# Performance work log

Hardware: AMD Instinct MI355X
Metric: run time of the kernel (lower is better)

## Reference

```python
import jax, jax.numpy as jnp
import numpy as np

N_NODES = 100000


def setup_inputs() -> dict:
    key = jax.random.key(0)
    k_x, k_e, k_w1, k_b1, k_w2, k_b2 = jax.random.split(key, 6)
    num_features, hidden, num_classes = 128, 64, 32
    x = jax.random.normal(k_x, (N_NODES, num_features), dtype=jnp.float32)
    edge_index = jax.random.randint(k_e, (2, 1600000), 0, N_NODES, dtype=jnp.int64)
    # torch.nn.Linear default init: U(-1/sqrt(fan_in), 1/sqrt(fan_in))
    s1 = 1.0 / np.sqrt(num_features)
    s2 = 1.0 / np.sqrt(hidden)
    W1 = jax.random.uniform(k_w1, (num_features, hidden), jnp.float32, -s1, s1)
    b1 = jax.random.uniform(k_b1, (hidden,), jnp.float32, -s1, s1)
    W2 = jax.random.uniform(k_w2, (hidden, num_classes), jnp.float32, -s2, s2)
    b2 = jax.random.uniform(k_b2, (num_classes,), jnp.float32, -s2, s2)
    return {"x": x, "edge_index": edge_index, "W1": W1, "b1": b1, "W2": W2, "b2": b2}


def reference(x, edge_index, W1, b1, W2, b2):
    # GNNConv: linear then scatter-add aggregation with self-loops
    xl = x @ W1 + b1                      # [N, hidden]
    src, dst = edge_index[0], edge_index[1]
    msgs = xl[src]                        # gather source features [E, hidden]
    agg = jax.ops.segment_sum(msgs, dst, num_segments=N_NODES)
    agg = agg + xl                        # add_self_loops contributes xl to each node
    h = jax.nn.relu(agg)
    return h @ W2 + b2                    # [N, num_classes]
```

## Files before the change

kernel.cpp:

```cpp
#include <hip/hip_runtime.h>
#include <hip/hip_bf16.h>

#define TPB 256
#define BSHIFT 7
#define BNODES (1 << BSHIFT)
#define NWRITERS 256

typedef int vint4 __attribute__((ext_vector_type(4)));
typedef __attribute__((ext_vector_type(8))) short short8v;
typedef __attribute__((ext_vector_type(4))) float f32x4;

__device__ __forceinline__ unsigned short f2bf(float f) {
    unsigned int u = __float_as_uint(f);
    u += 0x7fffu + ((u >> 16) & 1u);
    return (unsigned short)(u >> 16);
}
__device__ __forceinline__ float bflo(unsigned int u) { return __uint_as_float(u << 16); }
__device__ __forceinline__ float bfhi(unsigned int u) { return __uint_as_float(u & 0xffff0000u); }

__global__ __launch_bounds__(TPB) void k_gemm1_hist(
    const float* __restrict__ x, const float* __restrict__ W1, const float* __restrict__ b1,
    unsigned int* __restrict__ xlb,
    const int* __restrict__ ei, int* __restrict__ cntT,
    int N, int E, int NB, int CH)
{
    __shared__ unsigned short wT[64 * 136];
    __shared__ float b1s[64];
    __shared__ int   lcnt[1024];

    const int t = threadIdx.x;

    if ((int)blockIdx.x < NWRITERS) {
        const int hb = blockIdx.x;
        const int start = hb * CH;
        const int lim = min(E, start + CH);
        for (int j = t; j < NB; j += TPB) lcnt[j] = 0;
        __syncthreads();
        const int* dst = ei + E;
        int i = start + t * 4;
        for (; i + 3 < lim; i += TPB * 4) {
            vint4 d = __builtin_nontemporal_load(reinterpret_cast<const vint4*>(dst + i));
            atomicAdd(&lcnt[d.x >> BSHIFT], 1);
            atomicAdd(&lcnt[d.y >> BSHIFT], 1);
            atomicAdd(&lcnt[d.z >> BSHIFT], 1);
            atomicAdd(&lcnt[d.w >> BSHIFT], 1);
        }
        for (i = start + ((lim - start) & ~3) + t; i < lim; i += TPB)
            atomicAdd(&lcnt[dst[i] >> BSHIFT], 1);
        __syncthreads();
        for (int j = t; j < NB; j += TPB) cntT[j * NWRITERS + hb] = lcnt[j];
        return;
    }

    for (int i = t; i < 2048; i += TPB) {
        int k = i >> 4, cw = (i & 15) * 4;
        float4 u = reinterpret_cast<const float4*>(W1)[i];
        wT[(cw + 0) * 136 + k] = f2bf(u.x);
        wT[(cw + 1) * 136 + k] = f2bf(u.y);
        wT[(cw + 2) * 136 + k] = f2bf(u.z);
        wT[(cw + 3) * 136 + k] = f2bf(u.w);
    }
    if (t < 64) b1s[t] = b1[t];
    __syncthreads();

    const int l = t & 63, wid = t >> 6;
    const int cl = l & 15, kg = l >> 4;
    const int rw = ((int)blockIdx.x - NWRITERS) * 64 + wid * 16;
    if (rw >= N) return;
    const int r = rw + cl;

    const float4* xp4 = reinterpret_cast<const float4*>(x) + ((size_t)min(r, N - 1) * 32 + kg * 2);

    f32x4 acc[4] = {};
    #pragma unroll
    for (int kt = 0; kt < 4; ++kt) {
        float4 fA = xp4[kt * 8];
        float4 fB = xp4[kt * 8 + 1];
        short8v a;
        a[0] = (short)f2bf(fA.x); a[1] = (short)f2bf(fA.y);
        a[2] = (short)f2bf(fA.z); a[3] = (short)f2bf(fA.w);
        a[4] = (short)f2bf(fB.x); a[5] = (short)f2bf(fB.y);
        a[6] = (short)f2bf(fB.z); a[7] = (short)f2bf(fB.w);
        #pragma unroll
        for (int ct = 0; ct < 4; ++ct) {
            short8v b = *reinterpret_cast<const short8v*>(
                &wT[(ct * 16 + cl) * 136 + kt * 32 + kg * 8]);
            acc[ct] = __builtin_amdgcn_mfma_f32_16x16x32_bf16(a, b, acc[ct], 0, 0, 0);
        }
    }

    #pragma unroll
    for (int ct = 0; ct < 4; ++ct) {
        #pragma unroll
        for (int reg = 0; reg < 4; ++reg) {
            int row = rw + kg * 4 + reg;
            float v = acc[ct][reg] + b1s[ct * 16 + cl];
            unsigned int m = (unsigned int)f2bf(v);
            unsigned int p = (unsigned int)__shfl_xor((int)m, 1);
            if (!(l & 1) && row < N)
                xlb[(size_t)row * 32 + ct * 8 + (cl >> 1)] = m | (p << 16);
        }
    }
}

__global__ __launch_bounds__(TPB) void k_colscan(
    const int* __restrict__ cntT, int* __restrict__ segT, int* __restrict__ totals, int NB)
{
    __shared__ int wsum[4];
    const int r = blockIdx.x;
    const int t = threadIdx.x;
    const int lane = t & 63, wid = t >> 6;
    int v = cntT[r * NWRITERS + t];
    int incl = v;
    for (int d = 1; d < 64; d <<= 1) {
        int n = __shfl_up(incl, d);
        if (lane >= d) incl += n;
    }
    if (lane == 63) wsum[wid] = incl;
    __syncthreads();
    int woff = 0;
    for (int w = 0; w < wid; w++) woff += wsum[w];
    int excl = woff + incl - v;
    segT[r * NWRITERS + t] = excl;
    if (t == TPB - 1) totals[r] = excl + v;
}

__global__ void k_bucketbase(const int* __restrict__ totals, int* __restrict__ bb, int NB, int E)
{
    const int lane = threadIdx.x & 63;
    int carry = 0;
    for (int it = 0; it * 64 < NB; ++it) {
        int idx = it * 64 + lane;
        int v = (idx < NB) ? totals[idx] : 0;
        int incl = v;
        for (int d = 1; d < 64; d <<= 1) {
            int n = __shfl_up(incl, d);
            if (lane >= d) incl += n;
        }
        if (idx < NB) bb[idx] = carry + incl - v;
        carry += __shfl(incl, 63);
    }
    if (lane == 0) bb[NB] = E;
}

__global__ __launch_bounds__(TPB) void k_fillbin(
    const int* __restrict__ ei, const int* __restrict__ segT, const int* __restrict__ bb,
    unsigned int* __restrict__ recs, int E, int NB, int CH)
{
    __shared__ int lcur[1024];
    const int blk = blockIdx.x;
    const int t = threadIdx.x;
    for (int j = t; j < NB; j += TPB)
        lcur[j] = bb[j] + segT[j * NWRITERS + blk];
    __syncthreads();

    const int start = blk * CH;
    const int lim = min(E, start + CH);
    const int* src = ei;
    const int* dst = ei + E;
    int i = start + t * 4;
    for (; i + 3 < lim; i += TPB * 4) {
        vint4 d = __builtin_nontemporal_load(reinterpret_cast<const vint4*>(dst + i));
        vint4 s = __builtin_nontemporal_load(reinterpret_cast<const vint4*>(src + i));
        int p0 = atomicAdd(&lcur[d.x >> BSHIFT], 1);
        int p1 = atomicAdd(&lcur[d.y >> BSHIFT], 1);
        int p2 = atomicAdd(&lcur[d.z >> BSHIFT], 1);
        int p3 = atomicAdd(&lcur[d.w >> BSHIFT], 1);
        recs[p0] = ((unsigned int)s.x << BSHIFT) | (unsigned int)(d.x & (BNODES-1));
        recs[p1] = ((unsigned int)s.y << BSHIFT) | (unsigned int)(d.y & (BNODES-1));
        recs[p2] = ((unsigned int)s.z << BSHIFT) | (unsigned int)(d.z & (BNODES-1));
        recs[p3] = ((unsigned int)s.w << BSHIFT) | (unsigned int)(d.w & (BNODES-1));
    }
    for (i = start + ((lim - start) & ~3) + t; i < lim; i += TPB) {
        int d = dst[i];
        int p = atomicAdd(&lcur[d >> BSHIFT], 1);
        recs[p] = ((unsigned int)src[i] << BSHIFT) | (unsigned int)(d & (BNODES-1));
    }
}

__global__ __launch_bounds__(TPB) void k_bsort(
    const unsigned int* __restrict__ recs, const int* __restrict__ bb,
    int* __restrict__ esrc, int* __restrict__ off, int N, int NB, int E)
{
    __shared__ int h[BNODES];
    __shared__ int cur[BNODES];
    __shared__ int ws2[2];

    const int r = blockIdx.x;
    const int t = threadIdx.x;
    const int bb0 = bb[r], bb1 = bb[r + 1];

    if (t < BNODES) h[t] = 0;
    __syncthreads();
    for (int i = bb0 + t; i < bb1; i += TPB)
        atomicAdd(&h[recs[i] & (BNODES - 1)], 1);
    __syncthreads();

    int v = 0, incl = 0;
    const int lane = t & 63, w = t >> 6;
    if (t < BNODES) {
        v = h[t];
        incl = v;
        for (int d = 1; d < 64; d <<= 1) {
            int n = __shfl_up(incl, d);
            if (lane >= d) incl += n;
        }
        if (lane == 63) ws2[w] = incl;
    }
    __syncthreads();
    if (t < BNODES) {
        int excl = incl - v + (w ? ws2[0] : 0);
        cur[t] = bb0 + excl;
        int node = r * BNODES + t;
        if (node < N) off[node] = bb0 + excl;
    }
    if (r == NB - 1 && t == 0) off[N] = E;
    __syncthreads();

    for (int i = bb0 + t; i < bb1; i += TPB) {
        unsigned int rec = recs[i];
        int p = atomicAdd(&cur[rec & (BNODES - 1)], 1);
        esrc[p] = (int)(rec >> BSHIFT);
    }
}

#define AGG_BLOCKS 2048
__global__ __launch_bounds__(TPB) void k_agg(
    const unsigned int* __restrict__ xlb,
    const int* __restrict__ off,
    const int* __restrict__ esrc,
    const float* __restrict__ W2,
    const float* __restrict__ b2,
    float* __restrict__ out, int N)
{
    __shared__ float w2s[64 * 32];
    __shared__ float b2s[32];
    __shared__ float arow[4][68];

    const int t = threadIdx.x;
    const float4* w4 = reinterpret_cast<const float4*>(W2);
    for (int i = t; i < 512; i += TPB) {
        float4 u = w4[i];
        int o = i * 4;
        w2s[o+0] = u.x; w2s[o+1] = u.y; w2s[o+2] = u.z; w2s[o+3] = u.w;
    }
    if (t < 32) b2s[t] = b2[t];
    __syncthreads();

    const int wid = t >> 6, lane = t & 63;
    const int slot = lane >> 4, b = lane & 15;
    const int c = lane & 31, h = lane >> 5;
    const uint2* xb2 = reinterpret_cast<const uint2*>(xlb);

    for (int node = blockIdx.x * 4 + wid; node < N; node += gridDim.x * 4) {
        const int beg = off[node], end = off[node + 1];
        float a0 = 0.f, a1 = 0.f, a2 = 0.f, a3 = 0.f;
        int e = beg + slot;
        for (; e + 12 < end; e += 16) {
            int s0 = esrc[e], s1 = esrc[e + 4], s2 = esrc[e + 8], s3 = esrc[e + 12];
            uint2 v0 = xb2[(size_t)s0 * 16 + b];
            uint2 v1 = xb2[(size_t)s1 * 16 + b];
            uint2 v2 = xb2[(size_t)s2 * 16 + b];
            uint2 v3 = xb2[(size_t)s3 * 16 + b];
            a0 += bflo(v0.x); a1 += bfhi(v0.x); a2 += bflo(v0.y); a3 += bfhi(v0.y);
            a0 += bflo(v1.x); a1 += bfhi(v1.x); a2 += bflo(v1.y); a3 += bfhi(v1.y);
            a0 += bflo(v2.x); a1 += bfhi(v2.x); a2 += bflo(v2.y); a3 += bfhi(v2.y);
            a0 += bflo(v3.x); a1 += bfhi(v3.x); a2 += bflo(v3.y); a3 += bfhi(v3.y);
        }
        for (; e < end; e += 4) {
            uint2 v = xb2[(size_t)esrc[e] * 16 + b];
            a0 += bflo(v.x); a1 += bfhi(v.x); a2 += bflo(v.y); a3 += bfhi(v.y);
        }
        a0 += __shfl_xor(a0, 16); a1 += __shfl_xor(a1, 16);
        a2 += __shfl_xor(a2, 16); a3 += __shfl_xor(a3, 16);
        a0 += __shfl_xor(a0, 32); a1 += __shfl_xor(a1, 32);
        a2 += __shfl_xor(a2, 32); a3 += __shfl_xor(a3, 32);
        if (slot == 0) {
            uint2 sv = xb2[(size_t)node * 16 + b];
            float4 w;
            w.x = fmaxf(a0 + bflo(sv.x), 0.f);
            w.y = fmaxf(a1 + bfhi(sv.x), 0.f);
            w.z = fmaxf(a2 + bflo(sv.y), 0.f);
            w.w = fmaxf(a3 + bfhi(sv.y), 0.f);
            *reinterpret_cast<float4*>(&arow[wid][b * 4]) = w;
        }
        float o = 0.f;
        const float* ar = &arow[wid][h * 32];
        const float* wp = &w2s[h * 32 * 32 + c];
        #pragma unroll
        for (int kk = 0; kk < 32; kk++)
            o = fmaf(ar[kk], wp[kk * 32], o);
        o += __shfl_xor(o, 32);
        if (h == 0) out[(size_t)node * 32 + c] = o + b2s[c];
    }
}

extern "C" void kernel_launch(void* const* d_in, const int* in_sizes, int n_in,
                              void* d_out, int out_size, void* d_ws, size_t ws_size,
                              hipStream_t stream) {
    const float* x  = (const float*)d_in[0];
    const int*   ei = (const int*)d_in[1];
    const float* W1 = (const float*)d_in[2];
    const float* b1 = (const float*)d_in[3];
    const float* W2 = (const float*)d_in[4];
    const float* b2 = (const float*)d_in[5];
    float* out = (float*)d_out;

    const int N = in_sizes[0] / 128;
    const int E = in_sizes[1] / 2;
    const int NB = (N + BNODES - 1) >> BSHIFT;
    const int CH = (((E + NWRITERS - 1) / NWRITERS) + 3) & ~3;

    char* w = (char*)d_ws;
    unsigned int* xlb = (unsigned int*)w;   w += (size_t)N * 32 * 4;
    int* cntT   = (int*)w;                  w += (size_t)NB * NWRITERS * 4;
    int* segT   = (int*)w;                  w += (size_t)NB * NWRITERS * 4;
    int* totals = (int*)w;                  w += ((size_t)NB * 4 + 15) & ~15ull;
    int* bbase  = (int*)w;                  w += ((size_t)(NB + 1) * 4 + 15) & ~15ull;
    int* off    = (int*)w;                  w += ((size_t)(N + 1) * 4 + 15) & ~15ull;
    unsigned int* recs = (unsigned int*)w;  w += (size_t)E * 4;
    int* esrc   = (int*)w;

    const int nbG = (N + 63) / 64;

    hipLaunchKernelGGL(k_gemm1_hist, dim3(NWRITERS + nbG), dim3(TPB), 0, stream,
                       x, W1, b1, xlb, ei, cntT, N, E, NB, CH);
    hipLaunchKernelGGL(k_colscan, dim3(NB), dim3(TPB), 0, stream, cntT, segT, totals, NB);
    hipLaunchKernelGGL(k_bucketbase, dim3(1), dim3(64), 0, stream, totals, bbase, NB, E);
    hipLaunchKernelGGL(k_fillbin, dim3(NWRITERS), dim3(TPB), 0, stream,
                       ei, segT, bbase, recs, E, NB, CH);
    hipLaunchKernelGGL(k_bsort, dim3(NB), dim3(TPB), 0, stream,
                       recs, bbase, esrc, off, N, NB, E);
    hipLaunchKernelGGL(k_agg, dim3(AGG_BLOCKS), dim3(TPB), 0, stream,
                       xlb, off, esrc, W2, b2, out, N);
}
```

Baseline: 144.7 us.

## Fuse bucket sort into aggregation kernel using shared-memory sorted edge lists

Merges the per-bucket counting sort and the aggregation/second GEMM into one kernel per 128-node bucket. Sorted source indices stay in shared memory (up to 4096 edges) instead of being written to and re-read from global esrc/off arrays, which removes one launch and a global round trip. It also switches the gather to 16-byte loads with 8 lanes per row. Grid size drops from 2048 persistent blocks to one block per bucket, and large shared-memory use may lower occupancy; oversized buckets fall back to a slow full rescan of the bucket per node.

```diff
diff --git a/kernel.cpp b/kernel.cpp
--- a/kernel.cpp
+++ b/kernel.cpp
@@ -5,6 +5,7 @@
 #define BSHIFT 7
 #define BNODES (1 << BSHIFT)
 #define NWRITERS 256
+#define CAP 4096
 
 typedef int vint4 __attribute__((ext_vector_type(4)));
 typedef __attribute__((ext_vector_type(8))) short short8v;
@@ -178,66 +179,25 @@
     }
 }
 
-__global__ __launch_bounds__(TPB) void k_bsort(
+__global__ __launch_bounds__(TPB) void k_aggs(
     const unsigned int* __restrict__ recs, const int* __restrict__ bb,
-    int* __restrict__ esrc, int* __restrict__ off, int N, int NB, int E)
-{
-    __shared__ int h[BNODES];
-    __shared__ int cur[BNODES];
-    __shared__ int ws2[2];
-
-    const int r = blockIdx.x;
-    const int t = threadIdx.x;
-    const int bb0 = bb[r], bb1 = bb[r + 1];
-
-    if (t < BNODES) h[t] = 0;
-    __syncthreads();
-    for (int i = bb0 + t; i < bb1; i += TPB)
-        atomicAdd(&h[recs[i] & (BNODES - 1)], 1);
-    __syncthreads();
-
-    int v = 0, incl = 0;
-    const int lane = t & 63, w = t >> 6;
-    if (t < BNODES) {
-        v = h[t];
-        incl = v;
-        for (int d = 1; d < 64; d <<= 1) {
-            int n = __shfl_up(incl, d);
-            if (lane >= d) incl += n;
-        }
-        if (lane == 63) ws2[w] = incl;
-    }
-    __syncthreads();
-    if (t < BNODES) {
-        int excl = incl - v + (w ? ws2[0] : 0);
-        cur[t] = bb0 + excl;
-        int node = r * BNODES + t;
-        if (node < N) off[node] = bb0 + excl;
-    }
-    if (r == NB - 1 && t == 0) off[N] = E;
-    __syncthreads();
-
-    for (int i = bb0 + t; i < bb1; i += TPB) {
-        unsigned int rec = recs[i];
-        int p = atomicAdd(&cur[rec & (BNODES - 1)], 1);
-        esrc[p] = (int)(rec >> BSHIFT);
-    }
-}
-
-#define AGG_BLOCKS 2048
-__global__ __launch_bounds__(TPB) void k_agg(
     const unsigned int* __restrict__ xlb,
-    const int* __restrict__ off,
-    const int* __restrict__ esrc,
-    const float* __restrict__ W2,
-    const float* __restrict__ b2,
+    const float* __restrict__ W2, const float* __restrict__ b2,
     float* __restrict__ out, int N)
 {
+    __shared__ int   sorted[CAP];
     __shared__ float w2s[64 * 32];
     __shared__ float b2s[32];
+    __shared__ int   off[BNODES + 1];
+    __shared__ int   cur[BNODES];
+    __shared__ int   ws2[2];
     __shared__ float arow[4][68];
 
-    const int t = threadIdx.x;
+    const int r = blockIdx.x, t = threadIdx.x;
+    const int lane = t & 63, wid = t >> 6;
+    const int bb0 = bb[r], bb1 = bb[r + 1];
+    const int cr = bb1 - bb0;
+
     const float4* w4 = reinterpret_cast<const float4*>(W2);
     for (int i = t; i < 512; i += TPB) {
         float4 u = w4[i];
@@ -245,44 +205,105 @@
         w2s[o+0] = u.x; w2s[o+1] = u.y; w2s[o+2] = u.z; w2s[o+3] = u.w;
     }
     if (t < 32) b2s[t] = b2[t];
-    __syncthreads();
-
-    const int wid = t >> 6, lane = t & 63;
-    const int slot = lane >> 4, b = lane & 15;
+    if (t < BNODES) cur[t] = 0;
+    __syncthreads();
+
+    for (int i = bb0 + t; i < bb1; i += TPB)
+        atomicAdd(&cur[recs[i] & (BNODES - 1)], 1);
+    __syncthreads();
+
+    int v = 0, incl = 0;
+    if (t < BNODES) {
+        v = cur[t];
+        incl = v;
+        for (int d = 1; d < 64; d <<= 1) {
+            int n = __shfl_up(incl, d);
+            if (lane >= d) incl += n;
+        }
+        if (lane == 63) ws2[wid] = incl;
+    }
+    __syncthreads();
+    if (t < BNODES) {
+        int excl = incl - v + (wid ? ws2[0] : 0);
+        off[t] = excl;
+        cur[t] = excl;
+        if (t == BNODES - 1) off[BNODES] = cr;
+    }
+    __syncthreads();
+
+    const bool fits = (cr <= CAP);
+    if (fits) {
+        for (int i = bb0 + t; i < bb1; i += TPB) {
+            unsigned int rec = recs[i];
+            int p = atomicAdd(&cur[rec & (BNODES - 1)], 1);
+            sorted[p] = (int)(rec >> BSHIFT);
+        }
+    }
+    __syncthreads();
+
+    const int slot = lane >> 3, b = lane & 7;
     const int c = lane & 31, h = lane >> 5;
-    const uint2* xb2 = reinterpret_cast<const uint2*>(xlb);
-
-    for (int node = blockIdx.x * 4 + wid; node < N; node += gridDim.x * 4) {
-        const int beg = off[node], end = off[node + 1];
-        float a0 = 0.f, a1 = 0.f, a2 = 0.f, a3 = 0.f;
-        int e = beg + slot;
-        for (; e + 12 < end; e += 16) {
-            int s0 = esrc[e], s1 = esrc[e + 4], s2 = esrc[e + 8], s3 = esrc[e + 12];
-            uint2 v0 = xb2[(size_t)s0 * 16 + b];
-            uint2 v1 = xb2[(size_t)s1 * 16 + b];
-            uint2 v2 = xb2[(size_t)s2 * 16 + b];
-            uint2 v3 = xb2[(size_t)s3 * 16 + b];
-            a0 += bflo(v0.x); a1 += bfhi(v0.x); a2 += bflo(v0.y); a3 += bfhi(v0.y);
-            a0 += bflo(v1.x); a1 += bfhi(v1.x); a2 += bflo(v1.y); a3 += bfhi(v1.y);
-            a0 += bflo(v2.x); a1 += bfhi(v2.x); a2 += bflo(v2.y); a3 += bfhi(v2.y);
-            a0 += bflo(v3.x); a1 += bfhi(v3.x); a2 += bflo(v3.y); a3 += bfhi(v3.y);
-        }
-        for (; e < end; e += 4) {
-            uint2 v = xb2[(size_t)esrc[e] * 16 + b];
-            a0 += bflo(v.x); a1 += bfhi(v.x); a2 += bflo(v.y); a3 += bfhi(v.y);
-        }
-        a0 += __shfl_xor(a0, 16); a1 += __shfl_xor(a1, 16);
-        a2 += __shfl_xor(a2, 16); a3 += __shfl_xor(a3, 16);
-        a0 += __shfl_xor(a0, 32); a1 += __shfl_xor(a1, 32);
-        a2 += __shfl_xor(a2, 32); a3 += __shfl_xor(a3, 32);
+    const uint4* xb4 = reinterpret_cast<const uint4*>(xlb);
+
+    for (int dl = wid; dl < BNODES; dl += 4) {
+        const int node = r * BNODES + dl;
+        if (node >= N) break;
+        float a0=0.f,a1=0.f,a2=0.f,a3=0.f,a4=0.f,a5=0.f,a6=0.f,a7=0.f;
+        if (fits) {
+            const int beg = off[dl], end = off[dl + 1];
+            int e = beg + slot;
+            for (; e + 8 < end; e += 16) {
+                int s0 = sorted[e];
+                int s1 = sorted[e + 8];
+                uint4 v0 = xb4[(size_t)s0 * 8 + b];
+                uint4 v1 = xb4[(size_t)s1 * 8 + b];
+                a0 += bflo(v0.x); a1 += bfhi(v0.x);
+                a2 += bflo(v0.y); a3 += bfhi(v0.y);
+                a4 += bflo(v0.z); a5 += bfhi(v0.z);
+                a6 += bflo(v0.w); a7 += bfhi(v0.w);
+                a0 += bflo(v1.x); a1 += bfhi(v1.x);
+                a2 += bflo(v1.y); a3 += bfhi(v1.y);
+                a4 += bflo(v1.z); a5 += bfhi(v1.z);
+                a6 += bflo(v1.w); a7 += bfhi(v1.w);
+            }
+            if (e < end) {
+                int s = sorted[e];
+                uint4 vv = xb4[(size_t)s * 8 + b];
+                a0 += bflo(vv.x); a1 += bfhi(vv.x);
+                a2 += bflo(vv.y); a3 += bfhi(vv.y);
+                a4 += bflo(vv.z); a5 += bfhi(vv.z);
+                a6 += bflo(vv.w); a7 += bfhi(vv.w);
+            }
+        } else {
+            for (int i = bb0 + slot; i < bb1; i += 8) {
+                unsigned int rec = recs[i];
+                if ((int)(rec & (BNODES - 1)) == dl) {
+                    uint4 vv = xb4[(size_t)(rec >> BSHIFT) * 8 + b];
+                    a0 += bflo(vv.x); a1 += bfhi(vv.x);
+                    a2 += bflo(vv.y); a3 += bfhi(vv.y);
+                    a4 += bflo(vv.z); a5 += bfhi(vv.z);
+                    a6 += bflo(vv.w); a7 += bfhi(vv.w);
+                }
+            }
+        }
+        #pragma unroll
+        for (int d = 8; d <= 32; d <<= 1) {
+            a0 += __shfl_xor(a0, d); a1 += __shfl_xor(a1, d);
+            a2 += __shfl_xor(a2, d); a3 += __shfl_xor(a3, d);
+            a4 += __shfl_xor(a4, d); a5 += __shfl_xor(a5, d);
+            a6 += __shfl_xor(a6, d); a7 += __shfl_xor(a7, d);
+        }
         if (slot == 0) {
-            uint2 sv = xb2[(size_t)node * 16 + b];
-            float4 w;
-            w.x = fmaxf(a0 + bflo(sv.x), 0.f);
-            w.y = fmaxf(a1 + bfhi(sv.x), 0.f);
-            w.z = fmaxf(a2 + bflo(sv.y), 0.f);
-            w.w = fmaxf(a3 + bfhi(sv.y), 0.f);
-            *reinterpret_cast<float4*>(&arow[wid][b * 4]) = w;
+            uint4 sv = xb4[(size_t)node * 8 + b];
+            float* p = &arow[wid][b * 8];
+            p[0] = fmaxf(a0 + bflo(sv.x), 0.f);
+            p[1] = fmaxf(a1 + bfhi(sv.x), 0.f);
+            p[2] = fmaxf(a2 + bflo(sv.y), 0.f);
+            p[3] = fmaxf(a3 + bfhi(sv.y), 0.f);
+            p[4] = fmaxf(a4 + bflo(sv.z), 0.f);
+            p[5] = fmaxf(a5 + bfhi(sv.z), 0.f);
+            p[6] = fmaxf(a6 + bflo(sv.w), 0.f);
+            p[7] = fmaxf(a7 + bfhi(sv.w), 0.f);
         }
         float o = 0.f;
         const float* ar = &arow[wid][h * 32];
@@ -317,9 +338,7 @@
     int* segT   = (int*)w;                  w += (size_t)NB * NWRITERS * 4;
     int* totals = (int*)w;                  w += ((size_t)NB * 4 + 15) & ~15ull;
     int* bbase  = (int*)w;                  w += ((size_t)(NB + 1) * 4 + 15) & ~15ull;
-    int* off    = (int*)w;                  w += ((size_t)(N + 1) * 4 + 15) & ~15ull;
-    unsigned int* recs = (unsigned int*)w;  w += (size_t)E * 4;
-    int* esrc   = (int*)w;
+    unsigned int* recs = (unsigned int*)w;
 
     const int nbG = (N + 63) / 64;
 
@@ -329,8 +348,6 @@
     hipLaunchKernelGGL(k_bucketbase, dim3(1), dim3(64), 0, stream, totals, bbase, NB, E);
     hipLaunchKernelGGL(k_fillbin, dim3(NWRITERS), dim3(TPB), 0, stream,
                        ei, segT, bbase, recs, E, NB, CH);
-    hipLaunchKernelGGL(k_bsort, dim3(NB), dim3(TPB), 0, stream,
-                       recs, bbase, esrc, off, N, NB, E);
-    hipLaunchKernelGGL(k_agg, dim3(AGG_BLOCKS), dim3(TPB), 0, stream,
-                       xlb, off, esrc, W2, b2, out, N);
-}
+    hipLaunchKernelGGL(k_aggs, dim3(NB), dim3(TPB), 0, stream,
+                       recs, bbase, xlb, W2, b2, out, N);
+}
```

Result: no change. 142.7 us (-1.4%).
